# Kernel optimization log

Hardware: AMD Instinct MI355X
Metric: run time of the kernel (lower is better)

Reference implementation:

```python
import jax, jax.numpy as jnp
import numpy as np

C = 768
HEADS = 12
NF = 8      # num_frames
SL = 196    # seq_len (patches per frame)
B = 2
N = 1 + NF * SL
HID = 4 * C


def _ln(x, g, b, eps=1e-5):
    mu = jnp.mean(x, axis=-1, keepdims=True)
    var = jnp.mean((x - mu) ** 2, axis=-1, keepdims=True)
    return (x - mu) * jax.lax.rsqrt(var + eps) * g + b


def setup_inputs() -> dict:
    key = jax.random.key(0)
    ks = jax.random.split(key, 16)
    s = 0.02
    return {
        "x": jax.random.normal(ks[0], (B, N, C), jnp.float32),
        "g1": jnp.ones((C,), jnp.float32),
        "b1": jnp.zeros((C,), jnp.float32),
        "Wqkv": jax.random.normal(ks[1], (C, 3 * C), jnp.float32) * s,
        "Wq": jax.random.normal(ks[2], (C, C), jnp.float32) * s,
        "Wkv": jax.random.normal(ks[3], (C, 2 * C), jnp.float32) * s,
        "Wp": jax.random.normal(ks[4], (C, C), jnp.float32) * s,
        "bp": jnp.zeros((C,), jnp.float32),
        "g2": jnp.ones((C,), jnp.float32),
        "b2": jnp.zeros((C,), jnp.float32),
        "W1": jax.random.normal(ks[5], (C, HID), jnp.float32) * s,
        "bf1": jnp.zeros((HID,), jnp.float32),
        "W2": jax.random.normal(ks[6], (HID, C), jnp.float32) * s,
        "bf2": jnp.zeros((C,), jnp.float32),
        "seq_len": SL,
        "num_frames": NF,
    }


def _traj_attn(xn, Wqkv, Wq, Wkv, Wp, bp, P, F):
    Bb, Nn, Cc = xn.shape
    h = HEADS
    d = Cc // h
    scale = d ** -0.5
    S = F * P  # non-cls tokens

    qkv = xn @ Wqkv                                   # (B,N,3C)
    q, k, v = jnp.split(qkv, 3, axis=-1)

    def heads(t):  # (B,N,C) -> (B*h, N, d)
        return t.reshape(Bb, Nn, h, d).transpose(0, 2, 1, 3).reshape(Bb * h, Nn, d)

    q, k, v = heads(q), heads(k), heads(v)
    cls_q, q_ = q[:, :1], q[:, 1:]
    k_ = k[:, 1:]
    v_ = v[:, 1:]

    # cls token attends to all tokens
    sim = jnp.einsum('bid,bjd->bij', cls_q * scale, k)
    cls_out = jnp.einsum('bij,bjd->bid', jax.nn.softmax(sim, axis=-1), v)
    cls_out = cls_out.reshape(Bb, h, 1, d).transpose(0, 2, 1, 3).reshape(Bb, 1, Cc)

    # stage 1: space-only softmax per frame
    qk = jnp.einsum('bqd,bkd->bqk', q_, k_).reshape(Bb * h, S, F, P)
    space_attn = jax.nn.softmax(scale * qk, axis=-1)          # (Bh,S,F,P)
    v_r = v_.reshape(Bb * h, F, P, d)
    x1 = jnp.einsum('bqfn,bfnd->bqfd', space_attn, v_r)       # (Bh,S,F,d)
    x1 = x1.reshape(Bb, h, S, F, d).transpose(0, 2, 3, 1, 4).reshape(Bb, S, F, Cc)

    # diagonal across (query-frame, key-frame)
    xg = x1.reshape(Bb, F, P, F, Cc)
    diag = jnp.diagonal(xg, axis1=1, axis2=3)                 # (B,P,C,F)
    x_diag = diag.transpose(0, 3, 1, 2).reshape(Bb, S, Cc)    # b (f n) d

    # stage 2: frame-wise attention
    q2 = (x_diag @ Wq).reshape(Bb, S, h, d).transpose(0, 2, 1, 3) * scale  # bhsd
    kv2 = x1 @ Wkv
    k2, v2 = jnp.split(kv2, 2, axis=-1)
    k2 = k2.reshape(Bb, S, F, h, d).transpose(0, 3, 1, 2, 4)  # bhsfd
    attn2 = jax.nn.softmax(jnp.einsum('bhsd,bhsfd->bhsf', q2, k2), axis=-1)
    xo = x1.reshape(Bb, S, F, h, d).transpose(0, 3, 1, 2, 4)  # use_original_code=True
    out = jnp.einsum('bhsf,bhsfd->bhsd', attn2, xo)
    out = out.transpose(0, 2, 1, 3).reshape(Bb, S, Cc)

    out = jnp.concatenate([cls_out, out], axis=1) @ Wp + bp
    return out


def reference(x, g1, b1, Wqkv, Wq, Wkv, Wp, bp, g2, b2, W1, bf1, W2, bf2, seq_len, num_frames):
    x = x + _traj_attn(_ln(x, g1, b1), Wqkv, Wq, Wkv, Wp, bp, seq_len, num_frames)
    h = _ln(x, g2, b2)
    h = jax.nn.gelu(h @ W1 + bf1, approximate=False) @ W2 + bf2
    return x + h
```

## Files before the change

kernel.cpp:

```cpp
#include <hip/hip_runtime.h>
#include <hip/hip_bf16.h>
#include <math.h>

#define C     768
#define HEADS 12
#define HD    64
#define NF    8
#define SL    196
#define BB    2
#define NN    1569
#define SS    1568
#define HID   3072
#define CLS_CH 256
#define CLS_NC 7
#define QSCALE 0.18033688011112042f

typedef __attribute__((ext_vector_type(8))) short short8;
typedef __attribute__((ext_vector_type(4))) float f32x4;
typedef unsigned short u16;
typedef unsigned int u32;

__device__ inline float fast_exp2(float x) { return __builtin_amdgcn_exp2f(x); }

__device__ inline u16 f2b(float f) {
    __hip_bfloat16 h = __float2bfloat16(f);
    return *reinterpret_cast<u16*>(&h);
}
__device__ inline float b2f(u16 u) {
    union { unsigned u; float f; } v; v.u = ((unsigned)u) << 16;
    return v.f;
}

__device__ inline void gload_lds16(const void* g, void* l) {
    __builtin_amdgcn_global_load_lds(
        (const __attribute__((address_space(1))) void*)g,
        (__attribute__((address_space(3))) void*)l, 16, 0, 0);
}

__global__ void ln_kernel(const float* __restrict__ x, const float* __restrict__ g,
                          const float* __restrict__ b, u16* __restrict__ out, int rows) {
    int row = blockIdx.x;
    if (row >= rows) return;
    const float* xr = x + (size_t)row * C;
    int tid = threadIdx.x;
    float v[3];
    float sum = 0.f, sumsq = 0.f;
#pragma unroll
    for (int i = 0; i < 3; i++) {
        v[i] = xr[tid + 256 * i];
        sum += v[i]; sumsq += v[i] * v[i];
    }
    __shared__ float s1[4], s2[4];
    for (int off = 32; off; off >>= 1) {
        sum   += __shfl_xor(sum, off);
        sumsq += __shfl_xor(sumsq, off);
    }
    int wave = tid >> 6, lane = tid & 63;
    if (lane == 0) { s1[wave] = sum; s2[wave] = sumsq; }
    __syncthreads();
    sum   = s1[0] + s1[1] + s1[2] + s1[3];
    sumsq = s2[0] + s2[1] + s2[2] + s2[3];
    float mu  = sum / C;
    float var = sumsq / C - mu * mu;
    float rstd = rsqrtf(fmaxf(var, 0.f) + 1e-5f);
    u16* outr = out + (size_t)row * C;
#pragma unroll
    for (int i = 0; i < 3; i++) {
        int c = tid + 256 * i;
        outr[c] = f2b((v[i] - mu) * rstd * g[c] + b[c]);
    }
}

__global__ void wtrans_all_kernel(
    const float* __restrict__ Wqkv, const float* __restrict__ Wq,
    const float* __restrict__ Wkv,  const float* __restrict__ Wp,
    const float* __restrict__ W1,   const float* __restrict__ W2,
    u16* Tqkv, u16* Tq, u16* Tkv, u16* Tp, u16* T1, u16* T2) {
    __shared__ float tile[64][65];
    int bid = blockIdx.x;
    const float* W; u16* Wt; int K, ldb, gx;
    if (bid < 432)       { W = Wqkv; Wt = Tqkv; K = 768;  ldb = 2304; gx = 36; }
    else if (bid < 576)  { W = Wq;   Wt = Tq;   K = 768;  ldb = 768;  gx = 12; bid -= 432; }
    else if (bid < 720)  { W = Wkv;  Wt = Tkv;  K = 768;  ldb = 1536; gx = 12; bid -= 576; }
    else if (bid < 864)  { W = Wp;   Wt = Tp;   K = 768;  ldb = 768;  gx = 12; bid -= 720; }
    else if (bid < 1440) { W = W1;   Wt = T1;   K = 768;  ldb = 3072; gx = 48; bid -= 864; }
    else                 { W = W2;   Wt = T2;   K = 3072; ldb = 768;  gx = 12; bid -= 1440; }
    int nb = (bid % gx) * 64, kb = (bid / gx) * 64;
    int tx = threadIdx.x & 63, ty = threadIdx.x >> 6;
#pragma unroll
    for (int i = 0; i < 64; i += 4)
        tile[ty + i][tx] = W[(size_t)(kb + ty + i) * ldb + nb + tx];
    __syncthreads();
#pragma unroll
    for (int i = 0; i < 64; i += 4)
        Wt[(size_t)(nb + ty + i) * K + kb + tx] = f2b(tile[tx][ty + i]);
}

template<int MODE, int BM, int BN, int WAVES>
__global__ __launch_bounds__(WAVES * 64) void gemm_bf16(
    const u16* __restrict__ A, const u16* __restrict__ Bt,
    const float* __restrict__ bias, const float* resid, void* Cout,
    int M, int N, int K, int lda, int ldb, int gx) {
    constexpr int WCOLS = WAVES / 2;
    constexpr int WBN   = BN / WCOLS;
    constexpr int MT    = BM / 32;
    constexpr int NT    = WBN / 16;
    constexpr int ACH   = BM * 4;
    constexpr int TCH   = (BM + BN) * 4;
    constexpr int HALF  = (BM + BN) * 64;
    __shared__ char smem[2 * HALF];
    int tid = threadIdx.x, lane = tid & 63, wave = tid >> 6;
    int wr = wave / WCOLS, wc = wave % WCOLS;
    int r16 = lane & 15, kg = lane >> 4;

    int nwg = gridDim.x, orig = blockIdx.x;
    int qq = nwg >> 3, rr = nwg & 7, xcd = orig & 7, lid = orig >> 3;
    int wg = (xcd < rr ? xcd * (qq + 1) : rr * (qq + 1) + (xcd - rr) * qq) + lid;
    int bx = wg % gx, by = wg / gx;
    if constexpr (MODE == 4) {
        int mt_ = (M + BM - 1) / BM;
        int chunk = by / mt_; by -= chunk * mt_;
        A    += (size_t)chunk * K;
        Bt   += (size_t)chunk * K;
        Cout  = (void*)((float*)Cout + (size_t)chunk * ((size_t)M * N));
    }
    int row0 = by * BM, col0 = bx * BN;

    f32x4 acc[MT][NT];
#pragma unroll
    for (int mt = 0; mt < MT; mt++)
#pragma unroll
        for (int nt = 0; nt < NT; nt++) acc[mt][nt] = (f32x4){0.f, 0.f, 0.f, 0.f};

    auto stage = [&](char* dstbase, int ks) {
        int k0 = ks << 5;
#pragma unroll
        for (int it = 0; it < TCH / (WAVES * 64); it++) {
            int c = it * (WAVES * 64) + tid;
            const u16* src;
            if (c < ACH) {
                int ml = c >> 2, s = c & 3;
                int kgs = s ^ ((ml >> 1) & 3);
                int gm = row0 + ml; if (gm >= M) gm = M - 1;
                src = A + (size_t)gm * lda + k0 + kgs * 8;
            } else {
                int cc = c - ACH;
                int nl = cc >> 2, s = cc & 3;
                int kgs = s ^ ((nl >> 1) & 3);
                src = Bt + (size_t)(col0 + nl) * ldb + k0 + kgs * 8;
            }
            gload_lds16(src, dstbase + it * (WAVES * 1024) + wave * 1024);
        }
    };

    int nsteps = K >> 5;
    stage(smem, 0);
    __syncthreads();
    for (int ks = 0; ks < nsteps; ks++) {
        char* curb = smem + (ks & 1) * HALF;
        if (ks + 1 < nsteps) stage(smem + ((ks + 1) & 1) * HALF, ks + 1);
        short8 af[MT], bfr[NT];
#pragma unroll
        for (int mt = 0; mt < MT; mt++) {
            int ml = wr * (BM / 2) + mt * 16 + r16;
            af[mt] = *(const short8*)(curb + ml * 64 + ((kg ^ ((ml >> 1) & 3)) << 4));
        }
#pragma unroll
        for (int nt = 0; nt < NT; nt++) {
            int nl = wc * WBN + nt * 16 + r16;
            bfr[nt] = *(const short8*)(curb + BM * 64 + nl * 64 + ((kg ^ ((nl >> 1) & 3)) << 4));
        }
        __builtin_amdgcn_s_setprio(1);
#pragma unroll
        for (int mt = 0; mt < MT; mt++)
#pragma unroll
            for (int nt = 0; nt < NT; nt++)
                acc[mt][nt] = __builtin_amdgcn_mfma_f32_16x16x32_bf16(af[mt], bfr[nt], acc[mt][nt], 0, 0, 0);
        __builtin_amdgcn_s_setprio(0);
        __syncthreads();
    }
#pragma unroll
    for (int mt = 0; mt < MT; mt++) {
#pragma unroll
        for (int r2 = 0; r2 < 4; r2++) {
            int gm = row0 + wr * (BM / 2) + mt * 16 + kg * 4 + r2;
            if (gm >= M) continue;
#pragma unroll
            for (int nt = 0; nt < NT; nt++) {
                int gn = col0 + wc * WBN + nt * 16 + r16;
                float v = acc[mt][nt][r2];
                if constexpr (MODE == 1) {
                    v += bias[gn];
                    v = 0.5f * v * (1.f + erff(v * 0.70710678118f));
                }
                if constexpr (MODE == 2) {
                    v += bias[gn] + resid[(size_t)gm * N + gn];
                    ((float*)Cout)[(size_t)gm * N + gn] = v;
                } else if constexpr (MODE == 4) {
                    ((float*)Cout)[(size_t)gm * N + gn] = v;
                } else {
                    if constexpr (MODE == 3) { if (gn < 768) v *= QSCALE; }
                    ((u16*)Cout)[(size_t)gm * N + gn] = f2b(v);
                }
            }
        }
    }
}

__global__ void fc2_merge_kernel(const float* __restrict__ p,
                                 const float* __restrict__ bias, float* __restrict__ out) {
    int i = blockIdx.x * 256 + threadIdx.x;
    int total = BB * NN * (C / 4);
    if (i >= total) return;
    int c4 = i % (C / 4);
    size_t stride = (size_t)BB * NN * (C / 4);
    float4 bb = ((const float4*)bias)[c4];
    float4 a0 = ((const float4*)p)[i];
    float4 a1 = ((const float4*)p)[i + stride];
    float4 o  = ((float4*)out)[i];
    o.x += a0.x + a1.x + bb.x;
    o.y += a0.y + a1.y + bb.y;
    o.z += a0.z + a1.z + bb.z;
    o.w += a0.w + a1.w + bb.w;
    ((float4*)out)[i] = o;
}

__global__ void cls_partial_kernel(const u16* __restrict__ qkv, float* __restrict__ part) {
    int c = blockIdx.x, bh = blockIdx.y;
    int b = bh / HEADS, hh = bh % HEADS;
    int tid = threadIdx.x;
    int wave = tid >> 6, lane = tid & 63;
    __shared__ float s_q[HD];
    __shared__ float s_sc[CLS_CH];
    __shared__ float sm[4], ss[4];
    __shared__ float sacc[4][HD];
    if (tid < HD) s_q[tid] = b2f(qkv[(size_t)(b * NN) * 2304 + hh * HD + tid]);
    __syncthreads();

    int j0 = c * CLS_CH;
    int j = j0 + tid;
    float sc = -1e30f;
    if (j < NN) {
        const short8* kp = (const short8*)(qkv + ((size_t)(b * NN) + j) * 2304 + C + hh * HD);
        float acc = 0.f;
#pragma unroll
        for (int u = 0; u < 8; u++) {
            short8 kv = kp[u];
#pragma unroll
            for (int e = 0; e < 8; e++) acc += s_q[u * 8 + e] * b2f((u16)kv[e]);
        }
        sc = acc;
    }
    float m = sc;
    for (int off = 32; off; off >>= 1) m = fmaxf(m, __shfl_xor(m, off));
    if (lane == 0) sm[wave] = m;
    __syncthreads();
    m = fmaxf(fmaxf(sm[0], sm[1]), fmaxf(sm[2], sm[3]));
    float e = (j < NN) ? fast_exp2(sc - m) : 0.f;
    s_sc[tid] = e;
    float su = e;
    for (int off = 32; off; off >>= 1) su += __shfl_xor(su, off);
    if (lane == 0) ss[wave] = su;
    __syncthreads();
    float ssum = ss[0] + ss[1] + ss[2] + ss[3];

    int jj = tid >> 6, d = tid & 63;
    int jmax = NN - j0; if (jmax > CLS_CH) jmax = CLS_CH;
    const u16* vcol = qkv + ((size_t)(b * NN) + j0) * 2304 + 2 * C + hh * HD + d;
    float acc = 0.f;
    for (int t = jj; t < jmax; t += 4)
        acc += s_sc[t] * b2f(vcol[(size_t)t * 2304]);
    sacc[jj][d] = acc;
    __syncthreads();
    if (tid < HD) {
        float pv = sacc[0][tid] + sacc[1][tid] + sacc[2][tid] + sacc[3][tid];
        float* pp = part + ((size_t)bh * CLS_NC + c) * 66;
        pp[2 + tid] = pv;
        if (tid == 0) { pp[0] = m; pp[1] = ssum; }
    }
}

__global__ void cls_reduce_kernel(const float* __restrict__ part, u16* __restrict__ y) {
    int bh = blockIdx.x;
    int b = bh / HEADS, hh = bh % HEADS;
    int d = threadIdx.x;
    float gm = -1e30f;
#pragma unroll
    for (int c = 0; c < CLS_NC; c++)
        gm = fmaxf(gm, part[((size_t)bh * CLS_NC + c) * 66]);
    float tot = 0.f, pv = 0.f;
#pragma unroll
    for (int c = 0; c < CLS_NC; c++) {
        const float* pp = part + ((size_t)bh * CLS_NC + c) * 66;
        float w = fast_exp2(pp[0] - gm);
        tot += pp[1] * w;
        pv  += pp[2 + d] * w;
    }
    y[(size_t)(b * NN) * C + hh * HD + d] = f2b(pv / tot);
}

__global__ void repack_kv_kernel(const u16* __restrict__ qkv,
                                 u16* __restrict__ Kb, u16* __restrict__ Vt) {
    const int NK = 24 * NF * 208 * 8;
    const int NV = 24 * NF * 64 * 28;
    int t = blockIdx.x * 256 + threadIdx.x;
    if (t < NK) {
        int d8 = t & 7;
        int rest = t >> 3;
        int n = rest % 208;
        rest /= 208;
        int f = rest % NF;
        int bh = rest / NF;
        int b = bh / HEADS, h = bh % HEADS;
        short8 v = {0, 0, 0, 0, 0, 0, 0, 0};
        if (n < SL)
            v = *(const short8*)(qkv + ((size_t)(b * NN) + 1 + f * SL + n) * 2304 + C + h * HD + d8 * 8);
        *(short8*)(Kb + (((size_t)bh * NF + f) * 208 + n) * 64 + d8 * 8) = v;
    } else {
        int u = t - NK;
        if (u >= NV) return;
        int n8 = u % 28;
        int rest = u / 28;
        int d = rest % 64;
        rest /= 64;
        int f = rest % NF;
        int bh = rest / NF;
        int b = bh / HEADS, h = bh % HEADS;
        int n0 = n8 * 8;
        const u16* src = qkv + ((size_t)(b * NN) + 1 + f * SL) * 2304 + 2 * C + h * HD + d;
        short8 v;
#pragma unroll
        for (int jj = 0; jj < 8; jj++) {
            int n = n0 + jj;
            v[jj] = (n < SL) ? (short)src[(size_t)n * 2304] : (short)0;
        }
        *(short8*)(Vt + (((size_t)bh * NF + f) * 64 + d) * 224 + n0) = v;
    }
}

__global__ void space_attn_mfma(
    const u16* __restrict__ qkv, const u16* __restrict__ Kb,
    const u16* __restrict__ Vt, u16* __restrict__ x1, u16* __restrict__ xd) {
    __shared__ u16 smem[13312];
    int tid = threadIdx.x;
    int lane = tid & 63, wave = tid >> 6;
    int r16 = lane & 15, kg = lane >> 4;

    int n = blockIdx.x;
    int xcd = n & 7;
    int slot = n >> 3;
    int j = slot % 25;
    int gw = slot / 25;
    int bh = xcd * 3 + gw % 3;
    int f = gw / 3;
    int b = bh / HEADS, h = bh % HEADS;

    int strip = j * 4 + wave;
    bool act = strip < 98;
    if (!act) strip = 97;
    int q0 = strip * 16;

    const u16* qrow = qkv + ((size_t)(b * NN) + 1 + q0 + r16) * 2304 + h * HD + kg * 8;
    short8 aq0 = *(const short8*)(qrow);
    short8 aq1 = *(const short8*)(qrow + 32);

    const char* kb_g = (const char*)(Kb + ((size_t)bh * NF + f) * 208 * 64);
    for (int w = wave; w < 26; w += 4) {
        int p = w * 1024 + lane * 16;
        int row = p >> 7;
        int src = (p & ~127) | ((p & 127) ^ ((row & 7) << 4));
        gload_lds16(kb_g + src, (char*)smem + p);
    }
    __syncthreads();

    f32x4 acc[13];
#pragma unroll
    for (int t = 0; t < 13; t++) acc[t] = (f32x4){0.f, 0.f, 0.f, 0.f};
    const char* ksm = (const char*)smem;
    int swz = (r16 & 7) << 4;
    __builtin_amdgcn_s_setprio(1);
#pragma unroll
    for (int t = 0; t < 13; t++) {
        const char* krow = ksm + (t * 16 + r16) * 128;
        short8 bk0 = *(const short8*)(krow + ((kg * 16) ^ swz));
        short8 bk1 = *(const short8*)(krow + ((64 + kg * 16) ^ swz));
        acc[t] = __builtin_amdgcn_mfma_f32_16x16x32_bf16(bk0, aq0, acc[t], 0, 0, 0);
        acc[t] = __builtin_amdgcn_mfma_f32_16x16x32_bf16(bk1, aq1, acc[t], 0, 0, 0);
    }
    __builtin_amdgcn_s_setprio(0);

    const u16* vbase = Vt + ((size_t)bh * NF + f) * 64 * 224;
    short8 vf[2][4];
#pragma unroll
    for (int dt = 0; dt < 4; dt++)
        vf[0][dt] = *(const short8*)(vbase + (dt * 16 + r16) * 224 + kg * 8);

    bool tailz = (kg >= 1);
    float ssum = 0.f;
#pragma unroll
    for (int t = 0; t < 13; t++) {
#pragma unroll
        for (int r = 0; r < 4; r++) {
            float p = (t == 12 && tailz) ? 0.f : fast_exp2(acc[t][r]);
            acc[t][r] = p;
            ssum += p;
        }
    }
    ssum += __shfl_xor(ssum, 16);
    ssum += __shfl_xor(ssum, 32);
    float inv = 1.f / ssum;

    u32 w0[13], w1[13];
#pragma unroll
    for (int t = 0; t < 13; t++) {
        w0[t] = (u32)f2b(acc[t][0] * inv) | ((u32)f2b(acc[t][1] * inv) << 16);
        w1[t] = (u32)f2b(acc[t][2] * inv) | ((u32)f2b(acc[t][3] * inv) << 16);
    }

    int src0 = r16 + ((kg & 1) << 5);
    int src1 = src0 + 16;
    bool thi = (kg >= 2);
    f32x4 o[4];
#pragma unroll
    for (int dt = 0; dt < 4; dt++) o[dt] = (f32x4){0.f, 0.f, 0.f, 0.f};
    __builtin_amdgcn_s_setprio(1);
#pragma unroll
    for (int kc = 0; kc < 7; kc++) {
        if (kc < 6) {
#pragma unroll
            for (int dt = 0; dt < 4; dt++)
                vf[(kc + 1) & 1][dt] = *(const short8*)(vbase + (dt * 16 + r16) * 224 + (kc + 1) * 32 + kg * 8);
        }
        u32 s0, s1;
        if (kc == 6) { s0 = thi ? 0u : w0[12]; s1 = thi ? 0u : w1[12]; }
        else         { s0 = thi ? w0[2 * kc + 1] : w0[2 * kc];
                       s1 = thi ? w1[2 * kc + 1] : w1[2 * kc]; }
        union { u32 u[4]; short8 s8; } pau;
        pau.u[0] = (u32)__shfl((int)s0, src0);
        pau.u[1] = (u32)__shfl((int)s1, src0);
        pau.u[2] = (u32)__shfl((int)s0, src1);
        pau.u[3] = (u32)__shfl((int)s1, src1);
#pragma unroll
        for (int dt = 0; dt < 4; dt++)
            o[dt] = __builtin_amdgcn_mfma_f32_16x16x32_bf16(pau.s8, vf[kc & 1][dt], o[dt], 0, 0, 0);
    }
    __builtin_amdgcn_s_setprio(0);

    __syncthreads();
    if (act) {
        u16* eb = smem + wave * 1152;
#pragma unroll
        for (int dt = 0; dt < 4; dt++)
#pragma unroll
            for (int r = 0; r < 4; r++)
                eb[(kg * 4 + r) * 72 + dt * 16 + r16] = f2b(o[dt][r]);
        u16* x1row = x1 + (((size_t)(b * SS + q0)) * NF + f) * C + h * HD;
        u16* xdrow = xd + ((size_t)(b * SS + q0)) * C + h * HD;
        int fbase = f * SL;
#pragma unroll
        for (int it = 0; it < 2; it++) {
            int c = it * 64 + lane;
            int qr = c >> 3, c8 = c & 7;
            short8 v8 = *(const short8*)(&eb[qr * 72 + c8 * 8]);
            *(short8*)(x1row + (size_t)qr * (NF * C) + c8 * 8) = v8;
            if ((unsigned)(q0 + qr - fbase) < (unsigned)SL)
                *(short8*)(xdrow + (size_t)qr * C + c8 * 8) = v8;
        }
    }
}

__global__ void attn2_kernel(const u16* __restrict__ q2, const u16* __restrict__ k2,
                             const u16* __restrict__ x1, u16* __restrict__ y) {
    int item = blockIdx.x * 4 + (threadIdx.x >> 6);
    if (item >= BB * HEADS * SS) return;
    int lane = threadIdx.x & 63;
    int s = item % SS;
    int bh = item / SS;
    int b = bh / HEADS, hh = bh % HEADS;
    size_t rowbs = (size_t)(b * SS + s);
    float qv = b2f(q2[rowbs * C + hh * HD + lane]) * QSCALE;
    float lg[NF];
#pragma unroll
    for (int f = 0; f < NF; f++) {
        float p = qv * b2f(k2[(rowbs * NF + f) * C + hh * HD + lane]);
        for (int off = 32; off; off >>= 1) p += __shfl_xor(p, off);
        lg[f] = p;
    }
    float m = lg[0];
#pragma unroll
    for (int f = 1; f < NF; f++) m = fmaxf(m, lg[f]);
    float sum = 0.f;
#pragma unroll
    for (int f = 0; f < NF; f++) { lg[f] = fast_exp2(lg[f] - m); sum += lg[f]; }
    float inv = 1.f / sum;
    float acc = 0.f;
#pragma unroll
    for (int f = 0; f < NF; f++) acc += lg[f] * b2f(x1[(rowbs * NF + f) * C + hh * HD + lane]);
    y[((size_t)(b * NN) + 1 + s) * C + hh * HD + lane] = f2b(acc * inv);
}

extern "C" void kernel_launch(void* const* d_in, const int* in_sizes, int n_in,
                              void* d_out, int out_size, void* d_ws, size_t ws_size,
                              hipStream_t stream) {
    const float* x    = (const float*)d_in[0];
    const float* g1   = (const float*)d_in[1];
    const float* b1   = (const float*)d_in[2];
    const float* Wqkv = (const float*)d_in[3];
    const float* Wq   = (const float*)d_in[4];
    const float* Wkv  = (const float*)d_in[5];
    const float* Wp   = (const float*)d_in[6];
    const float* bp   = (const float*)d_in[7];
    const float* g2   = (const float*)d_in[8];
    const float* b2_  = (const float*)d_in[9];
    const float* W1   = (const float*)d_in[10];
    const float* bf1  = (const float*)d_in[11];
    const float* W2   = (const float*)d_in[12];
    const float* bf2  = (const float*)d_in[13];
    float* out = (float*)d_out;

    u16* us     = (u16*)d_ws;
    u16* xn_b   = us;
    u16* qkv_b  = xn_b   + 2409984;
    u16* Wt_qkv = qkv_b  + 7229952;
    u16* Wt_q   = Wt_qkv + 1769472;
    u16* Wt_kv  = Wt_q   + 589824;
    u16* Wt_p   = Wt_kv  + 589824;
    u16* W1t    = Wt_p   + 589824;
    u16* W2t    = W1t    + 2359296;
    u16* Kb     = W2t    + 2359296;
    u16* Vt     = Kb     + 2555904;
    u16* x1b    = Vt     + 2752512;
    u16* xdb    = x1b    + 19267584;
    u16* q2b    = xdb    + 2408448;
    u16* k2b    = q2b    + 2408448;
    u16* y_b    = k2b    + 19267584;
    u16* a1b    = y_b    + 2409984;
    float* cls_ws   = (float*)(a1b + 9639936);
    float* fc2_part = cls_ws + 24 * 7 * 66;

    const int M1 = BB * NN;
    const int M2 = BB * SS;
    const int M3 = BB * SS * NF;

    wtrans_all_kernel<<<2016, 256, 0, stream>>>(Wqkv, Wq, Wkv, Wp, W1, W2,
                                                Wt_qkv, Wt_q, Wt_kv, Wt_p, W1t, W2t);
    ln_kernel<<<M1, 256, 0, stream>>>(x, g1, b1, xn_b, M1);
    gemm_bf16<3, 128, 128, 8><<<18 * 25, 512, 0, stream>>>(
        xn_b, Wt_qkv, nullptr, nullptr, qkv_b, M1, 2304, 768, 768, 768, 18);
    repack_kv_kernel<<<(24 * NF * 208 * 8 + 24 * NF * 64 * 28 + 255) / 256, 256, 0, stream>>>(
        qkv_b, Kb, Vt);
    cls_partial_kernel<<<dim3(CLS_NC, BB * HEADS), 256, 0, stream>>>(qkv_b, cls_ws);
    cls_reduce_kernel<<<BB * HEADS, 64, 0, stream>>>(cls_ws, y_b);
    space_attn_mfma<<<4800, 256, 0, stream>>>(qkv_b, Kb, Vt, x1b, xdb);
    gemm_bf16<0, 64, 64, 4><<<12 * 49, 256, 0, stream>>>(
        xdb, Wt_q, nullptr, nullptr, q2b, M2, 768, 768, 768, 768, 12);
    gemm_bf16<0, 128, 128, 8><<<6 * 196, 512, 0, stream>>>(
        x1b, Wt_kv, nullptr, nullptr, k2b, M3, 768, 768, 768, 768, 6);
    attn2_kernel<<<(BB * HEADS * SS + 3) / 4, 256, 0, stream>>>(q2b, k2b, x1b, y_b);
    gemm_bf16<2, 64, 64, 4><<<12 * 50, 256, 0, stream>>>(
        y_b, Wt_p, bp, x, out, M1, 768, 768, 768, 768, 12);
    ln_kernel<<<M1, 256, 0, stream>>>(out, g2, b2_, xn_b, M1);
    gemm_bf16<1, 128, 128, 8><<<24 * 25, 512, 0, stream>>>(
        xn_b, W1t, bf1, nullptr, a1b, M1, 3072, 768, 768, 768, 24);
    gemm_bf16<4, 128, 64, 4><<<12 * 25 * 2, 256, 0, stream>>>(
        a1b, W2t, nullptr, nullptr, fc2_part, M1, 768, 1536, 3072, 3072, 12);
    fc2_merge_kernel<<<(BB * NN * (C / 4) + 255) / 256, 256, 0, stream>>>(
        fc2_part, bf2, out);
}
```

Measured before the change: 278.0 us.

## Process two query strips per wave in space attention to reuse K/V

```diff
diff --git a/kernel.cpp b/kernel.cpp
--- a/kernel.cpp
+++ b/kernel.cpp
@@ -349,20 +349,23 @@
     int n = blockIdx.x;
     int xcd = n & 7;
     int slot = n >> 3;
-    int j = slot % 25;
-    int gw = slot / 25;
+    int j = slot % 13;
+    int gw = slot / 13;
     int bh = xcd * 3 + gw % 3;
     int f = gw / 3;
     int b = bh / HEADS, h = bh % HEADS;
 
-    int strip = j * 4 + wave;
-    bool act = strip < 98;
-    if (!act) strip = 97;
-    int q0 = strip * 16;
-
-    const u16* qrow = qkv + ((size_t)(b * NN) + 1 + q0 + r16) * 2304 + h * HD + kg * 8;
-    short8 aq0 = *(const short8*)(qrow);
-    short8 aq1 = *(const short8*)(qrow + 32);
+    int sA = j * 8 + wave * 2, sB = sA + 1;
+    bool actA = sA < 98, actB = sB < 98;
+    int q0A = (actA ? sA : 97) * 16;
+    int q0B = (actB ? sB : 97) * 16;
+
+    const u16* qrowA = qkv + ((size_t)(b * NN) + 1 + q0A + r16) * 2304 + h * HD + kg * 8;
+    const u16* qrowB = qkv + ((size_t)(b * NN) + 1 + q0B + r16) * 2304 + h * HD + kg * 8;
+    short8 aqA0 = *(const short8*)(qrowA);
+    short8 aqA1 = *(const short8*)(qrowA + 32);
+    short8 aqB0 = *(const short8*)(qrowB);
+    short8 aqB1 = *(const short8*)(qrowB + 32);
 
     const char* kb_g = (const char*)(Kb + ((size_t)bh * NF + f) * 208 * 64);
     for (int w = wave; w < 26; w += 4) {
@@ -373,56 +376,88 @@
     }
     __syncthreads();
 
-    f32x4 acc[13];
-#pragma unroll
-    for (int t = 0; t < 13; t++) acc[t] = (f32x4){0.f, 0.f, 0.f, 0.f};
     const char* ksm = (const char*)smem;
     int swz = (r16 & 7) << 4;
+    bool tailz = (kg >= 1);
+    const u16* vbase = Vt + ((size_t)bh * NF + f) * 64 * 224;
+
+    f32x4 acc[13];
+    u32 w0A[13], w1A[13], w0B[13], w1B[13];
+
+#pragma unroll
+    for (int t = 0; t < 13; t++) acc[t] = (f32x4){0.f, 0.f, 0.f, 0.f};
     __builtin_amdgcn_s_setprio(1);
 #pragma unroll
     for (int t = 0; t < 13; t++) {
         const char* krow = ksm + (t * 16 + r16) * 128;
         short8 bk0 = *(const short8*)(krow + ((kg * 16) ^ swz));
         short8 bk1 = *(const short8*)(krow + ((64 + kg * 16) ^ swz));
-        acc[t] = __builtin_amdgcn_mfma_f32_16x16x32_bf16(bk0, aq0, acc[t], 0, 0, 0);
-        acc[t] = __builtin_amdgcn_mfma_f32_16x16x32_bf16(bk1, aq1, acc[t], 0, 0, 0);
+        acc[t] = __builtin_amdgcn_mfma_f32_16x16x32_bf16(bk0, aqA0, acc[t], 0, 0, 0);
+        acc[t] = __builtin_amdgcn_mfma_f32_16x16x32_bf16(bk1, aqA1, acc[t], 0, 0, 0);
     }
     __builtin_amdgcn_s_setprio(0);
-
-    const u16* vbase = Vt + ((size_t)bh * NF + f) * 64 * 224;
     short8 vf[2][4];
 #pragma unroll
     for (int dt = 0; dt < 4; dt++)
         vf[0][dt] = *(const short8*)(vbase + (dt * 16 + r16) * 224 + kg * 8);
-
-    bool tailz = (kg >= 1);
-    float ssum = 0.f;
+    {
+        float ssum = 0.f;
+#pragma unroll
+        for (int t = 0; t < 13; t++)
+#pragma unroll
+            for (int r = 0; r < 4; r++) {
+                float p = (t == 12 && tailz) ? 0.f : fast_exp2(acc[t][r]);
+                acc[t][r] = p;
+                ssum += p;
+            }
+        ssum += __shfl_xor(ssum, 16);
+        ssum += __shfl_xor(ssum, 32);
+        float inv = 1.f / ssum;
+#pragma unroll
+        for (int t = 0; t < 13; t++) {
+            w0A[t] = (u32)f2b(acc[t][0] * inv) | ((u32)f2b(acc[t][1] * inv) << 16);
+            w1A[t] = (u32)f2b(acc[t][2] * inv) | ((u32)f2b(acc[t][3] * inv) << 16);
+        }
+    }
+
+#pragma unroll
+    for (int t = 0; t < 13; t++) acc[t] = (f32x4){0.f, 0.f, 0.f, 0.f};
+    __builtin_amdgcn_s_setprio(1);
 #pragma unroll
     for (int t = 0; t < 13; t++) {
-#pragma unroll
-        for (int r = 0; r < 4; r++) {
-            float p = (t == 12 && tailz) ? 0.f : fast_exp2(acc[t][r]);
-            acc[t][r] = p;
-            ssum += p;
-        }
-    }
-    ssum += __shfl_xor(ssum, 16);
-    ssum += __shfl_xor(ssum, 32);
-    float inv = 1.f / ssum;
-
-    u32 w0[13], w1[13];
-#pragma unroll
-    for (int t = 0; t < 13; t++) {
-        w0[t] = (u32)f2b(acc[t][0] * inv) | ((u32)f2b(acc[t][1] * inv) << 16);
-        w1[t] = (u32)f2b(acc[t][2] * inv) | ((u32)f2b(acc[t][3] * inv) << 16);
+        const char* krow = ksm + (t * 16 + r16) * 128;
+        short8 bk0 = *(const short8*)(krow + ((kg * 16) ^ swz));
+        short8 bk1 = *(const short8*)(krow + ((64 + kg * 16) ^ swz));
+        acc[t] = __builtin_amdgcn_mfma_f32_16x16x32_bf16(bk0, aqB0, acc[t], 0, 0, 0);
+        acc[t] = __builtin_amdgcn_mfma_f32_16x16x32_bf16(bk1, aqB1, acc[t], 0, 0, 0);
+    }
+    __builtin_amdgcn_s_setprio(0);
+    {
+        float ssum = 0.f;
+#pragma unroll
+        for (int t = 0; t < 13; t++)
+#pragma unroll
+            for (int r = 0; r < 4; r++) {
+                float p = (t == 12 && tailz) ? 0.f : fast_exp2(acc[t][r]);
+                acc[t][r] = p;
+                ssum += p;
+            }
+        ssum += __shfl_xor(ssum, 16);
+        ssum += __shfl_xor(ssum, 32);
+        float inv = 1.f / ssum;
+#pragma unroll
+        for (int t = 0; t < 13; t++) {
+            w0B[t] = (u32)f2b(acc[t][0] * inv) | ((u32)f2b(acc[t][1] * inv) << 16);
+            w1B[t] = (u32)f2b(acc[t][2] * inv) | ((u32)f2b(acc[t][3] * inv) << 16);
+        }
     }
 
     int src0 = r16 + ((kg & 1) << 5);
     int src1 = src0 + 16;
     bool thi = (kg >= 2);
-    f32x4 o[4];
-#pragma unroll
-    for (int dt = 0; dt < 4; dt++) o[dt] = (f32x4){0.f, 0.f, 0.f, 0.f};
+    f32x4 oA[4], oB[4];
+#pragma unroll
+    for (int dt = 0; dt < 4; dt++) { oA[dt] = (f32x4){0.f, 0.f, 0.f, 0.f}; oB[dt] = (f32x4){0.f, 0.f, 0.f, 0.f}; }
     __builtin_amdgcn_s_setprio(1);
 #pragma unroll
     for (int kc = 0; kc < 7; kc++) {
@@ -431,39 +466,67 @@
             for (int dt = 0; dt < 4; dt++)
                 vf[(kc + 1) & 1][dt] = *(const short8*)(vbase + (dt * 16 + r16) * 224 + (kc + 1) * 32 + kg * 8);
         }
-        u32 s0, s1;
-        if (kc == 6) { s0 = thi ? 0u : w0[12]; s1 = thi ? 0u : w1[12]; }
-        else         { s0 = thi ? w0[2 * kc + 1] : w0[2 * kc];
-                       s1 = thi ? w1[2 * kc + 1] : w1[2 * kc]; }
-        union { u32 u[4]; short8 s8; } pau;
-        pau.u[0] = (u32)__shfl((int)s0, src0);
-        pau.u[1] = (u32)__shfl((int)s1, src0);
-        pau.u[2] = (u32)__shfl((int)s0, src1);
-        pau.u[3] = (u32)__shfl((int)s1, src1);
-#pragma unroll
-        for (int dt = 0; dt < 4; dt++)
-            o[dt] = __builtin_amdgcn_mfma_f32_16x16x32_bf16(pau.s8, vf[kc & 1][dt], o[dt], 0, 0, 0);
+        u32 a0, a1, b0, b1;
+        if (kc == 6) {
+            a0 = thi ? 0u : w0A[12]; a1 = thi ? 0u : w1A[12];
+            b0 = thi ? 0u : w0B[12]; b1 = thi ? 0u : w1B[12];
+        } else {
+            a0 = thi ? w0A[2 * kc + 1] : w0A[2 * kc];
+            a1 = thi ? w1A[2 * kc + 1] : w1A[2 * kc];
+            b0 = thi ? w0B[2 * kc + 1] : w0B[2 * kc];
+            b1 = thi ? w1B[2 * kc + 1] : w1B[2 * kc];
+        }
+        union { u32 u[4]; short8 s8; } pA, pB;
+        pA.u[0] = (u32)__shfl((int)a0, src0);
+        pA.u[1] = (u32)__shfl((int)a1, src0);
+        pA.u[2] = (u32)__shfl((int)a0, src1);
+        pA.u[3] = (u32)__shfl((int)a1, src1);
+        pB.u[0] = (u32)__shfl((int)b0, src0);
+        pB.u[1] = (u32)__shfl((int)b1, src0);
+        pB.u[2] = (u32)__shfl((int)b0, src1);
+        pB.u[3] = (u32)__shfl((int)b1, src1);
+#pragma unroll
+        for (int dt = 0; dt < 4; dt++) {
+            oA[dt] = __builtin_amdgcn_mfma_f32_16x16x32_bf16(pA.s8, vf[kc & 1][dt], oA[dt], 0, 0, 0);
+            oB[dt] = __builtin_amdgcn_mfma_f32_16x16x32_bf16(pB.s8, vf[kc & 1][dt], oB[dt], 0, 0, 0);
+        }
     }
     __builtin_amdgcn_s_setprio(0);
 
     __syncthreads();
-    if (act) {
-        u16* eb = smem + wave * 1152;
-#pragma unroll
-        for (int dt = 0; dt < 4; dt++)
-#pragma unroll
-            for (int r = 0; r < 4; r++)
-                eb[(kg * 4 + r) * 72 + dt * 16 + r16] = f2b(o[dt][r]);
-        u16* x1row = x1 + (((size_t)(b * SS + q0)) * NF + f) * C + h * HD;
-        u16* xdrow = xd + ((size_t)(b * SS + q0)) * C + h * HD;
-        int fbase = f * SL;
+    u16* ebA = smem + wave * 2304;
+    u16* ebB = ebA + 1152;
+    int fbase = f * SL;
+#pragma unroll
+    for (int dt = 0; dt < 4; dt++)
+#pragma unroll
+        for (int r = 0; r < 4; r++) {
+            ebA[(kg * 4 + r) * 72 + dt * 16 + r16] = f2b(oA[dt][r]);
+            ebB[(kg * 4 + r) * 72 + dt * 16 + r16] = f2b(oB[dt][r]);
+        }
+    if (actA) {
+        u16* x1row = x1 + (((size_t)(b * SS + q0A)) * NF + f) * C + h * HD;
+        u16* xdrow = xd + ((size_t)(b * SS + q0A)) * C + h * HD;
 #pragma unroll
         for (int it = 0; it < 2; it++) {
             int c = it * 64 + lane;
             int qr = c >> 3, c8 = c & 7;
-            short8 v8 = *(const short8*)(&eb[qr * 72 + c8 * 8]);
+            short8 v8 = *(const short8*)(&ebA[qr * 72 + c8 * 8]);
             *(short8*)(x1row + (size_t)qr * (NF * C) + c8 * 8) = v8;
-            if ((unsigned)(q0 + qr - fbase) < (unsigned)SL)
+            if ((unsigned)(q0A + qr - fbase) < (unsigned)SL)
+                *(short8*)(xdrow + (size_t)qr * C + c8 * 8) = v8;
+        }
+    }
+    if (actB) {
+        u16* x1row = x1 + (((size_t)(b * SS + q0B)) * NF + f) * C + h * HD;
+        u16* xdrow = xd + ((size_t)(b * SS + q0B)) * C + h * HD;
+#pragma unroll
+        for (int it = 0; it < 2; it++) {
+            int c = it * 64 + lane;
+            int qr = c >> 3, c8 = c & 7;
+            short8 v8 = *(const short8*)(&ebB[qr * 72 + c8 * 8]);
+            *(short8*)(x1row + (size_t)qr * (NF * C) + c8 * 8) = v8;
+            if ((unsigned)(q0B + qr - fbase) < (unsigned)SL)
                 *(short8*)(xdrow + (size_t)qr * C + c8 * 8) = v8;
         }
     }
@@ -551,7 +614,7 @@
         qkv_b, Kb, Vt);
     cls_partial_kernel<<<dim3(CLS_NC, BB * HEADS), 256, 0, stream>>>(qkv_b, cls_ws);
     cls_reduce_kernel<<<BB * HEADS, 64, 0, stream>>>(cls_ws, y_b);
-    space_attn_mfma<<<4800, 256, 0, stream>>>(qkv_b, Kb, Vt, x1b, xdb);
+    space_attn_mfma<<<2496, 256, 0, stream>>>(qkv_b, Kb, Vt, x1b, xdb);
     gemm_bf16<0, 64, 64, 4><<<12 * 49, 256, 0, stream>>>(
         xdb, Wt_q, nullptr, nullptr, q2b, M2, 768, 768, 768, 768, 12);
     gemm_bf16<0, 128, 128, 8><<<6 * 196, 512, 0, stream>>>(
```

Result: faster. 269.4 us (-3.1%).
